# Kernel tuning notes

Hardware: AMD Instinct MI355X
Metric: run time of the kernel (lower is better)

## Reference

```python
import jax, jax.numpy as jnp
import numpy as np

N_EMBD = 1024
N_HEAD = 16
HEAD = N_EMBD // N_HEAD


def setup_inputs() -> dict:
    key = jax.random.key(0)
    ks = jax.random.split(key, 6)
    B, S = 4, 2048
    scale = 1.0 / np.sqrt(N_EMBD)
    return {
        "x": jax.random.normal(ks[0], (B, S, N_EMBD), dtype=jnp.float32),
        "Wq": jax.random.normal(ks[1], (N_EMBD, N_EMBD), dtype=jnp.float32) * scale,
        "Wk": jax.random.normal(ks[2], (N_EMBD, N_EMBD), dtype=jnp.float32) * scale,
        "Wv": jax.random.normal(ks[3], (N_EMBD, N_EMBD), dtype=jnp.float32) * scale,
        "Wo": jax.random.normal(ks[4], (N_EMBD, N_EMBD), dtype=jnp.float32) * scale,
        "bo": jnp.zeros((N_EMBD,), dtype=jnp.float32),
    }


def reference(x, Wq, Wk, Wv, Wo, bo):
    B, S, _ = x.shape
    # projections; nn.Linear applies x @ W.T but W is random here, so x @ W is equivalent math
    def split_heads(t):  # (B,S,E) -> (B,H,S,D)
        return t.reshape(B, S, N_HEAD, HEAD).transpose(0, 2, 1, 3)

    q = split_heads(x @ Wq)
    k = split_heads(x @ Wk)
    v = split_heads(x @ Wv)
    scores = jnp.einsum("bhqd,bhkd->bhqk", q, k) * (HEAD ** -0.5)
    causal = jnp.tril(jnp.ones((S, S), dtype=bool))
    scores = jnp.where(causal, scores, -jnp.inf)
    weights = jax.nn.softmax(scores, axis=-1)  # dropout p=0 (eval)
    out = jnp.einsum("bhqk,bhkd->bhqd", weights, v)
    out = out.transpose(0, 2, 1, 3).reshape(B, S, N_EMBD)
    return out @ Wo + bo
```

## Files before the change

kernel.cpp:

```cpp
#include <hip/hip_runtime.h>
#include <hip/hip_bf16.h>

typedef unsigned short u16;
typedef unsigned int u32;
typedef __bf16 bf16x8 __attribute__((ext_vector_type(8)));
typedef float f32x4 __attribute__((ext_vector_type(4)));
typedef u16 u16x8 __attribute__((ext_vector_type(8)));
typedef u16 u16x4 __attribute__((ext_vector_type(4)));

#define NB 4
#define SEQ 2048
#define EMB 1024
#define NHEAD 16
#define DHEAD 64
#define MTOT (NB*SEQ)

static __device__ __forceinline__ u16 f2bf(float f) {
  union { __bf16 h; u16 u; } cv;
  cv.h = (__bf16)f;
  return cv.u;
}

static __device__ __forceinline__ float fexp2(float x) {
  float r;
  asm("v_exp_f32 %0, %1" : "=v"(r) : "v"(x));
  return r;
}

static __device__ __forceinline__ void gload16(const void* g, void* l) {
  __builtin_amdgcn_global_load_lds((const __attribute__((address_space(1))) void*)g,
                                   (__attribute__((address_space(3))) void*)l, 16, 0, 0);
}


__global__ __launch_bounds__(256) void k_cvt_x(const float* __restrict__ in, u16* __restrict__ out) {
  size_t i = (size_t)blockIdx.x * 256 + threadIdx.x;
  const float4* p = (const float4*)in + i * 2;
  float4 a = p[0], b = p[1];
  u16x8 r;
  r[0] = f2bf(a.x); r[1] = f2bf(a.y); r[2] = f2bf(a.z); r[3] = f2bf(a.w);
  r[4] = f2bf(b.x); r[5] = f2bf(b.y); r[6] = f2bf(b.z); r[7] = f2bf(b.w);
  *(u16x8*)(out + i * 8) = r;
}

__global__ __launch_bounds__(256) void k_wtrans(const float* __restrict__ W0, const float* __restrict__ W1,
                                                const float* __restrict__ W2, const float* __restrict__ W3,
                                                u16* __restrict__ O0, u16* __restrict__ O1,
                                                u16* __restrict__ O2, u16* __restrict__ O3) {
  __shared__ float tile[64][65];
  const float* W = blockIdx.z == 0 ? W0 : blockIdx.z == 1 ? W1 : blockIdx.z == 2 ? W2 : W3;
  u16* O       = blockIdx.z == 0 ? O0 : blockIdx.z == 1 ? O1 : blockIdx.z == 2 ? O2 : O3;
  const int c0 = blockIdx.x * 64, r0 = blockIdx.y * 64;
  const int t = threadIdx.x;
  const int tr = t >> 4, tc = (t & 15) * 4;
#pragma unroll
  for (int p = 0; p < 4; p++) {
    int r = tr + p * 16;
    float4 v = *(const float4*)&W[(size_t)(r0 + r) * EMB + c0 + tc];
    tile[r][tc + 0] = v.x; tile[r][tc + 1] = v.y; tile[r][tc + 2] = v.z; tile[r][tc + 3] = v.w;
  }
  __syncthreads();
#pragma unroll
  for (int p = 0; p < 4; p++) {
    int orow = tr + p * 16;
    u16x4 o;
    o[0] = f2bf(tile[tc + 0][orow]); o[1] = f2bf(tile[tc + 1][orow]);
    o[2] = f2bf(tile[tc + 2][orow]); o[3] = f2bf(tile[tc + 3][orow]);
    *(u16x4*)&O[(size_t)(c0 + orow) * EMB + r0 + tc] = o;
  }
}


static __device__ __forceinline__ void gemm_core(const u16* __restrict__ A, const u16* __restrict__ BT,
                                                 int m0, int n0, f32x4 acc[4][4]) {
  __shared__ u16 As[2][128 * 64];
  __shared__ u16 Bs[2][128 * 64];
  const int t = threadIdx.x, l = t & 63, w = t >> 6;
  const int g = l >> 4, q = l & 15;
  const int wm = (w >> 1) * 64, wn = (w & 1) * 64;

  const f32x4 zero4 = {0.f, 0.f, 0.f, 0.f};
#pragma unroll
  for (int mi = 0; mi < 4; mi++)
#pragma unroll
    for (int ni = 0; ni < 4; ni++) acc[mi][ni] = zero4;

  int srow[4], skel[4];
#pragma unroll
  for (int i = 0; i < 4; i++) {
    int row = w * 32 + i * 8 + (l >> 3);
    srow[i] = row; skel[i] = ((l & 7) ^ (row & 7)) * 8;
  }

  auto stage = [&](int k0, int bsel) {
    char* AsB = (char*)As[bsel] + w * 4096;
    char* BsB = (char*)Bs[bsel] + w * 4096;
#pragma unroll
    for (int i = 0; i < 4; i++) {
      gload16(A + (size_t)(m0 + srow[i]) * EMB + k0 + skel[i], AsB + i * 1024);
      gload16(BT + (size_t)(n0 + srow[i]) * EMB + k0 + skel[i], BsB + i * 1024);
    }
  };

  auto compute = [&](int bsel) {
    char* AsB = (char*)As[bsel];
    char* BsB = (char*)Bs[bsel];
#pragma unroll
    for (int kc = 0; kc < 2; kc++) {
      bf16x8 af[4], bfv[4];
#pragma unroll
      for (int mi = 0; mi < 4; mi++) {
        int row = wm + mi * 16 + q;
        af[mi] = *(const bf16x8*)(AsB + row * 128 + (((kc * 4 + g) ^ (row & 7)) << 4));
      }
#pragma unroll
      for (int ni = 0; ni < 4; ni++) {
        int row = wn + ni * 16 + q;
        bfv[ni] = *(const bf16x8*)(BsB + row * 128 + (((kc * 4 + g) ^ (row & 7)) << 4));
      }
      __builtin_amdgcn_s_setprio(1);
#pragma unroll
      for (int mi = 0; mi < 4; mi++)
#pragma unroll
        for (int ni = 0; ni < 4; ni++)
          acc[mi][ni] = __builtin_amdgcn_mfma_f32_16x16x32_bf16(af[mi], bfv[ni], acc[mi][ni], 0, 0, 0);
      __builtin_amdgcn_s_setprio(0);
    }
  };

  stage(0, 0);
  int buf = 0;
  for (int k0 = 64; k0 <= EMB; k0 += 64) {
    const bool pf = (k0 < EMB);
    if (pf) {
      stage(k0, buf ^ 1);
      asm volatile("s_waitcnt vmcnt(8)" ::: "memory");
    } else {
      asm volatile("s_waitcnt vmcnt(0)" ::: "memory");
    }
    __builtin_amdgcn_s_barrier();
    __builtin_amdgcn_sched_barrier(0);
    compute(buf);
    asm volatile("s_waitcnt lgkmcnt(0)" ::: "memory");
    __builtin_amdgcn_s_barrier();
    buf ^= 1;
  }
}

__global__ __launch_bounds__(512, 2) void k_gemm_qkv(const u16* __restrict__ xb, const u16* __restrict__ Wqkv,
                                                     u16* __restrict__ Qb, u16* __restrict__ Kb, u16* __restrict__ Vb) {
  __shared__ u16 As[2][256 * 64];
  __shared__ u16 Bs[2][256 * 64];
  const int t = threadIdx.x, l = t & 63, wid = t >> 6;
  const int g = l >> 4, q = l & 15;
  const int wr = wid >> 2, wc = wid & 3;

  const int wg = blockIdx.x;
  const int c = wg & 7, local = wg >> 3;
  const int idx = c * 48 + local;
  const int ni_ = idx >> 5, mi_ = idx & 31;
  const int m0 = mi_ * 256, n0 = ni_ * 256;

  f32x4 acc[2][2][4][2];
  const f32x4 zero4 = {0.f, 0.f, 0.f, 0.f};
#pragma unroll
  for (int R = 0; R < 2; R++)
#pragma unroll
    for (int C = 0; C < 2; C++)
#pragma unroll
      for (int mi = 0; mi < 4; mi++)
#pragma unroll
        for (int ni = 0; ni < 2; ni++) acc[R][C][mi][ni] = zero4;

  int srow[2], skel[2];
#pragma unroll
  for (int j = 0; j < 2; j++) {
    int row = j * 64 + (t >> 3);
    srow[j] = row; skel[j] = ((t & 7) ^ (row & 7)) * 8;
  }

  auto stageHalf = [&](int op, int half, int tile) {
    if (tile >= 16) return;
    const int kk = tile * 64, d = tile & 1;
    const u16* src = op ? Wqkv : xb;
    const int base = op ? n0 : m0;
    char* dst = (char*)(op ? Bs[d] : As[d]) + half * 16384 + wid * 1024;
#pragma unroll
    for (int j = 0; j < 2; j++)
      gload16(src + (size_t)(base + half * 128 + srow[j]) * EMB + kk + skel[j], dst + j * 8192);
  };

  bf16x8 af[4][2], bf0[2][2], bf1[2][2];
  auto loadA = [&](int R, int d) {
    char* Ab = (char*)As[d];
#pragma unroll
    for (int mi = 0; mi < 4; mi++)
#pragma unroll
      for (int kc = 0; kc < 2; kc++) {
        int row = R * 128 + wr * 64 + mi * 16 + q;
        af[mi][kc] = *(const bf16x8*)(Ab + row * 128 + (((kc * 4 + g) ^ (row & 7)) << 4));
      }
  };
  auto loadB = [&](int C, int d, bf16x8 (&bfv)[2][2]) {
    char* Bb = (char*)Bs[d];
#pragma unroll
    for (int ni = 0; ni < 2; ni++)
#pragma unroll
      for (int kc = 0; kc < 2; kc++) {
        int row = C * 128 + wc * 32 + ni * 16 + q;
        bfv[ni][kc] = *(const bf16x8*)(Bb + row * 128 + (((kc * 4 + g) ^ (row & 7)) << 4));
      }
  };

#define MFMA16(R, C, BF)                                                                   \
  do {                                                                                     \
    __builtin_amdgcn_s_setprio(1);                                                         \
    _Pragma("unroll")                                                                      \
    for (int kc = 0; kc < 2; kc++)                                                         \
      _Pragma("unroll")                                                                    \
      for (int mi = 0; mi < 4; mi++)                                                       \
        _Pragma("unroll")                                                                  \
        for (int ni = 0; ni < 2; ni++)                                                     \
          acc[R][C][mi][ni] = __builtin_amdgcn_mfma_f32_16x16x32_bf16(af[mi][kc], BF[ni][kc], acc[R][C][mi][ni], 0, 0, 0); \
    __builtin_amdgcn_s_setprio(0);                                                         \
  } while (0)

  stageHalf(0, 0, 0); stageHalf(1, 0, 0); stageHalf(1, 1, 0); stageHalf(0, 1, 0);
  stageHalf(0, 0, 1); stageHalf(1, 1, 1);
  asm volatile("s_waitcnt vmcnt(4)" ::: "memory");
  __builtin_amdgcn_s_barrier();
  __builtin_amdgcn_sched_barrier(0);

  for (int kt = 0; kt < 16; ++kt) {
    const int d = kt & 1;
    loadA(0, d); loadB(0, d, bf0);
    stageHalf(0, 1, kt + 1);
    __builtin_amdgcn_s_barrier();
    MFMA16(0, 0, bf0);
    __builtin_amdgcn_s_barrier();
    __builtin_amdgcn_sched_barrier(0);
    loadB(1, d, bf1);
    stageHalf(1, 0, kt + 1);
    __builtin_amdgcn_s_barrier();
    MFMA16(0, 1, bf1);
    __builtin_amdgcn_s_barrier();
    __builtin_amdgcn_sched_barrier(0);
    loadA(1, d);
    stageHalf(0, 0, kt + 2);
    __builtin_amdgcn_s_barrier();
    MFMA16(1, 1, bf1);
    __builtin_amdgcn_s_barrier();
    __builtin_amdgcn_sched_barrier(0);
    stageHalf(1, 1, kt + 2);
    __builtin_amdgcn_s_barrier();
    MFMA16(1, 0, bf0);
    if (kt <= 13)      asm volatile("s_waitcnt vmcnt(4)" ::: "memory");
    else if (kt == 14) asm volatile("s_waitcnt vmcnt(0)" ::: "memory");
    __builtin_amdgcn_s_barrier();
    __builtin_amdgcn_sched_barrier(0);
  }
#undef MFMA16

  const int z = n0 >> 10;
  u16* Out = z == 0 ? Qb : (z == 1 ? Kb : Vb);
  const float scale = z == 0 ? 0.125f * 1.4426950408889634f : 1.0f;

#pragma unroll
  for (int R = 0; R < 2; R++)
#pragma unroll
    for (int C = 0; C < 2; C++)
#pragma unroll
      for (int mi = 0; mi < 4; mi++)
#pragma unroll
        for (int ni = 0; ni < 2; ni++)
#pragma unroll
          for (int jj = 0; jj < 4; jj++) {
            int m = m0 + R * 128 + wr * 64 + mi * 16 + g * 4 + jj;
            int n = n0 + C * 128 + wc * 32 + ni * 16 + q;
            int b = m >> 11, s = m & 2047;
            int col = n & 1023;
            int h = col >> 6, dd = col & 63;
            Out[(((size_t)(b * NHEAD + h)) * SEQ + s) * DHEAD + dd] = f2bf(acc[R][C][mi][ni][jj] * scale);
          }
}

__global__ __launch_bounds__(256) void k_gemm_out(const u16* __restrict__ Ob, const u16* __restrict__ WoT,
                                                  const float* __restrict__ bo, float* __restrict__ out) {
  const int wg = blockIdx.x;
  const int c = wg & 7, local = wg >> 3;
  const int m0 = (local & 63) * 128, n0 = c * 128;

  f32x4 acc[4][4];
  gemm_core(Ob, WoT, m0, n0, acc);

  const int t = threadIdx.x, l = t & 63, w = t >> 6;
  const int g = l >> 4, q = l & 15;
  const int wm = (w >> 1) * 64, wn = (w & 1) * 64;
#pragma unroll
  for (int ni = 0; ni < 4; ni++) {
    int n = n0 + wn + ni * 16 + q;
    float bv = bo[n];
#pragma unroll
    for (int mi = 0; mi < 4; mi++)
#pragma unroll
      for (int jj = 0; jj < 4; jj++) {
        int m = m0 + wm + mi * 16 + g * 4 + jj;
        out[(size_t)m * EMB + n] = acc[mi][ni][jj] + bv;
      }
  }
}

__global__ __launch_bounds__(256, 4) void k_attn(const u16* __restrict__ Qb, const u16* __restrict__ Kb,
                                                 const u16* __restrict__ Vb, u16* __restrict__ Ob) {
  __shared__ u16 Ks[2][64 * 64];
  __shared__ u16 Vt[2][64 * 64];
  const int t = threadIdx.x, l = t & 63, w = t >> 6;
  const int g = l >> 4, q = l & 15;
  const int bh = blockIdx.x;
  const int b = bh >> 4, h = bh & 15;
  const size_t hb = (size_t)bh * SEQ * DHEAD;
  const float NEG_INF = -__builtin_inff();

  const int i = blockIdx.y;
  const int qA0 = i * 64, qB0 = (31 - i) * 64;
  const int ntA = i + 1, ntB = 32 - i;

  int krow[2], kel[2];
#pragma unroll
  for (int ii = 0; ii < 2; ii++) {
    int row = w * 16 + ii * 8 + (l >> 3);
    krow[ii] = row; kel[ii] = ((l & 7) ^ (row & 7)) * 8;
  }
  const int kp = t & 31, d0v = (t >> 5) * 8;
  const int r2 = 2 * kp;
  const int sp = 32 * ((r2 >> 4) >> 1) + 8 * ((r2 >> 2) & 3) + 4 * ((r2 >> 4) & 1) + (r2 & 3);

  int olds[2][4], owv[8];
#pragma unroll
  for (int kc = 0; kc < 2; kc++)
#pragma unroll
    for (int kf = 0; kf < 4; kf++) {
      int row = kf * 16 + q;
      olds[kc][kf] = row * 128 + (((kc * 4 + g) ^ (row & 7)) << 4);
    }
#pragma unroll
  for (int ii = 0; ii < 8; ii++) {
    int d = d0v + ii;
    owv[ii] = d * 128 + ((sp * 2) ^ ((d & 7) << 4));
  }

  const u16* kgp0 = Kb + hb + (size_t)krow[0] * DHEAD + kel[0];
  const u16* kgp1 = Kb + hb + (size_t)krow[1] * DHEAD + kel[1];
  const u16* vgp0 = Vb + hb + (size_t)(2 * kp) * DHEAD + d0v;
  const u16* vgp1 = vgp0 + DHEAD;

  auto stageK = [&](const u16* p0, const u16* p1, int bsel) {
    char* dst = (char*)Ks[bsel] + w * 2048;
    gload16(p0, dst);
    gload16(p1, dst + 1024);
  };
  auto writeV = [&](int bsel, const u16x8& v0, const u16x8& v1) {
    char* VtB = (char*)Vt[bsel];
#pragma unroll
    for (int ii = 0; ii < 8; ii++) {
      u32 val = (u32)v0[ii] | ((u32)v1[ii] << 16);
      *(u32*)(VtB + owv[ii]) = val;
    }
  };

  bf16x8 qfA[2], qfB[2];
#pragma unroll
  for (int kc = 0; kc < 2; kc++) {
    qfA[kc] = *(const bf16x8*)(Qb + hb + (size_t)(qA0 + w * 16 + q) * DHEAD + kc * 32 + g * 8);
    qfB[kc] = *(const bf16x8*)(Qb + hb + (size_t)(qB0 + w * 16 + q) * DHEAD + kc * 32 + g * 8);
  }
  const int qglobA = qA0 + w * 16 + q, qglobB = qB0 + w * 16 + q;

  f32x4 oA[4], oB[4];
  const f32x4 zero4 = {0.f, 0.f, 0.f, 0.f};
#pragma unroll
  for (int df = 0; df < 4; df++) { oA[df] = zero4; oB[df] = zero4; }
  float mA = NEG_INF, lA = 0.f, mB = NEG_INF, lB = 0.f;

  auto compute = [&](const bf16x8 (&qf)[2], f32x4 (&o)[4], float& m_run, float& l_run,
                     bool diag, int qglob, int k0, const char* KsB, const char* VtB) {
    f32x4 st[4];
#pragma unroll
    for (int kf = 0; kf < 4; kf++) st[kf] = zero4;
    __builtin_amdgcn_s_setprio(1);
#pragma unroll
    for (int kc = 0; kc < 2; kc++)
#pragma unroll
      for (int kf = 0; kf < 4; kf++) {
        bf16x8 a = *(const bf16x8*)(KsB + olds[kc][kf]);
        st[kf] = __builtin_amdgcn_mfma_f32_16x16x32_bf16(a, qf[kc], st[kf], 0, 0, 0);
      }
    __builtin_amdgcn_s_setprio(0);

    if (diag) {
#pragma unroll
      for (int kf = 0; kf < 4; kf++)
#pragma unroll
        for (int jj = 0; jj < 4; jj++)
          if (k0 + kf * 16 + g * 4 + jj > qglob) st[kf][jj] = NEG_INF;
    }

    float x0 = fmaxf(fmaxf(st[0][0], st[0][1]), st[0][2]);
    float x1 = fmaxf(fmaxf(st[0][3], st[1][0]), st[1][1]);
    float x2 = fmaxf(fmaxf(st[1][2], st[1][3]), st[2][0]);
    float x3 = fmaxf(fmaxf(st[2][1], st[2][2]), st[2][3]);
    float x4 = fmaxf(fmaxf(st[3][0], st[3][1]), st[3][2]);
    float smax = fmaxf(fmaxf(x0, x1), x2);
    smax = fmaxf(fmaxf(smax, x3), x4);
    smax = fmaxf(smax, st[3][3]);
    smax = fmaxf(smax, __shfl_xor(smax, 16));
    smax = fmaxf(smax, __shfl_xor(smax, 32));

    if (!__all(smax - m_run <= 8.0f)) {
      float mnew = fmaxf(m_run, smax);
      float sc = fexp2(m_run - mnew);
      l_run *= sc;
#pragma unroll
      for (int jj = 0; jj < 4; jj++) {
        float scj = __shfl(sc, g * 4 + jj);
#pragma unroll
        for (int df = 0; df < 4; df++) o[df][jj] *= scj;
      }
      m_run = mnew;
    }

    f32x4 pv[4];
#pragma unroll
    for (int kf = 0; kf < 4; kf++)
#pragma unroll
      for (int jj = 0; jj < 4; jj++)
        pv[kf][jj] = fexp2(st[kf][jj] - m_run);
    f32x4 sv = (pv[0] + pv[1]) + (pv[2] + pv[3]);
    l_run += (sv[0] + sv[1]) + (sv[2] + sv[3]);

    bf16x8 pa[2];
    pa[0] = bf16x8{ (__bf16)pv[0][0], (__bf16)pv[0][1], (__bf16)pv[0][2], (__bf16)pv[0][3],
                    (__bf16)pv[1][0], (__bf16)pv[1][1], (__bf16)pv[1][2], (__bf16)pv[1][3] };
    pa[1] = bf16x8{ (__bf16)pv[2][0], (__bf16)pv[2][1], (__bf16)pv[2][2], (__bf16)pv[2][3],
                    (__bf16)pv[3][0], (__bf16)pv[3][1], (__bf16)pv[3][2], (__bf16)pv[3][3] };

    __builtin_amdgcn_s_setprio(1);
#pragma unroll
    for (int kc = 0; kc < 2; kc++)
#pragma unroll
      for (int df = 0; df < 4; df++) {
        bf16x8 vb = *(const bf16x8*)(VtB + olds[kc][df]);
        o[df] = __builtin_amdgcn_mfma_f32_16x16x32_bf16(pa[kc], vb, o[df], 0, 0, 0);
      }
    __builtin_amdgcn_s_setprio(0);
  };

  {
    u16x8 v0 = *(const u16x8*)vgp0, v1 = *(const u16x8*)vgp1;
    stageK(kgp0, kgp1, 0);
    writeV(0, v0, v1);
    kgp0 += 4096; kgp1 += 4096; vgp0 += 4096; vgp1 += 4096;
  }
  __syncthreads();

  int buf = 0;
  for (int kt = 0; kt < ntB; ++kt) {
    const int k0 = kt * 64;
    const bool pf = (kt + 1 < ntB);
    u16x8 nv0, nv1;
    if (pf) {
      stageK(kgp0, kgp1, buf ^ 1);
      nv0 = *(const u16x8*)vgp0; nv1 = *(const u16x8*)vgp1;
      kgp0 += 4096; kgp1 += 4096; vgp0 += 4096; vgp1 += 4096;
    }
    const char* KsB = (const char*)Ks[buf];
    const char* VtB = (const char*)Vt[buf];

    compute(qfB, oB, mB, lB, kt == ntB - 1, qglobB, k0, KsB, VtB);
    __builtin_amdgcn_sched_barrier(0);
    if (kt < ntA)
      compute(qfA, oA, mA, lA, kt == ntA - 1, qglobA, k0, KsB, VtB);

    if (pf) writeV(buf ^ 1, nv0, nv1);
    __syncthreads();
    buf ^= 1;
  }

  lA += __shfl_xor(lA, 16); lA += __shfl_xor(lA, 32);
  lB += __shfl_xor(lB, 16); lB += __shfl_xor(lB, 32);

  auto store = [&](f32x4 (&o)[4], float l_run, int q0) {
    float inv = 1.f / l_run;
#pragma unroll
    for (int jj = 0; jj < 4; jj++) {
      float r = __shfl(inv, g * 4 + jj);
      int s = q0 + w * 16 + g * 4 + jj;
#pragma unroll
      for (int df = 0; df < 4; df++)
        Ob[((size_t)(b * SEQ + s)) * EMB + h * DHEAD + df * 16 + q] = f2bf(o[df][jj] * r);
    }
  };
  store(oA, lA, qA0);
  store(oB, lB, qB0);
}


extern "C" void kernel_launch(void* const* d_in, const int* in_sizes, int n_in,
                              void* d_out, int out_size, void* d_ws, size_t ws_size,
                              hipStream_t stream) {
  const float* x  = (const float*)d_in[0];
  const float* Wq = (const float*)d_in[1];
  const float* Wk = (const float*)d_in[2];
  const float* Wv = (const float*)d_in[3];
  const float* Wo = (const float*)d_in[4];
  const float* bo = (const float*)d_in[5];
  float* out = (float*)d_out;

  char* ws = (char*)d_ws;
  u16* xb  = (u16*)(ws);
  u16* WqT = (u16*)(ws + (16u << 20));
  u16* WkT = WqT + (size_t)EMB * EMB;
  u16* WvT = WkT + (size_t)EMB * EMB;
  u16* WoT = WvT + (size_t)EMB * EMB;
  u16* Qb  = (u16*)(ws + (24u << 20));
  u16* Kb  = Qb + (size_t)MTOT * EMB;
  u16* Vb  = Kb + (size_t)MTOT * EMB;
  u16* Ob  = Vb + (size_t)MTOT * EMB;

  k_cvt_x<<<dim3(4096), 256, 0, stream>>>(x, xb);
  k_wtrans<<<dim3(16, 16, 4), 256, 0, stream>>>(Wq, Wk, Wv, Wo, WqT, WkT, WvT, WoT);
  k_gemm_qkv<<<dim3(384), 512, 0, stream>>>(xb, WqT, Qb, Kb, Vb);
  k_attn<<<dim3(64, 16), 256, 0, stream>>>(Qb, Kb, Vb, Ob);
  k_gemm_out<<<dim3(512), 256, 0, stream>>>(Ob, WoT, bo, out);
}
```

Baseline: 165.5 us.

## Share K/V LDS fragment loads across both query blocks in attention loop

Restructures the per-tile attention step so that the QK^T MMAs for both query blocks (A and B) run together using the same K fragments loaded once from LDS. Both softmaxes are then computed, followed by PV MMAs for both blocks using shared V fragments. This halves LDS reads of K/V per tile and interleaves more independent MFMAs. In exchange it raises register pressure, since two sets of score and probability fragments are live at once, and it removes the sched_barrier that separated the two blocks.

```diff
diff --git a/kernel.cpp b/kernel.cpp
--- a/kernel.cpp
+++ b/kernel.cpp
@@ -382,21 +382,8 @@
   for (int df = 0; df < 4; df++) { oA[df] = zero4; oB[df] = zero4; }
   float mA = NEG_INF, lA = 0.f, mB = NEG_INF, lB = 0.f;
 
-  auto compute = [&](const bf16x8 (&qf)[2], f32x4 (&o)[4], float& m_run, float& l_run,
-                     bool diag, int qglob, int k0, const char* KsB, const char* VtB) {
-    f32x4 st[4];
-#pragma unroll
-    for (int kf = 0; kf < 4; kf++) st[kf] = zero4;
-    __builtin_amdgcn_s_setprio(1);
-#pragma unroll
-    for (int kc = 0; kc < 2; kc++)
-#pragma unroll
-      for (int kf = 0; kf < 4; kf++) {
-        bf16x8 a = *(const bf16x8*)(KsB + olds[kc][kf]);
-        st[kf] = __builtin_amdgcn_mfma_f32_16x16x32_bf16(a, qf[kc], st[kf], 0, 0, 0);
-      }
-    __builtin_amdgcn_s_setprio(0);
-
+  auto softmax_pa = [&](f32x4 (&st)[4], f32x4 (&o)[4], float& m_run, float& l_run,
+                        bool diag, int qglob, int k0, bf16x8 (&pa)[2]) {
     if (diag) {
 #pragma unroll
       for (int kf = 0; kf < 4; kf++)
@@ -438,21 +425,10 @@
     f32x4 sv = (pv[0] + pv[1]) + (pv[2] + pv[3]);
     l_run += (sv[0] + sv[1]) + (sv[2] + sv[3]);
 
-    bf16x8 pa[2];
     pa[0] = bf16x8{ (__bf16)pv[0][0], (__bf16)pv[0][1], (__bf16)pv[0][2], (__bf16)pv[0][3],
                     (__bf16)pv[1][0], (__bf16)pv[1][1], (__bf16)pv[1][2], (__bf16)pv[1][3] };
     pa[1] = bf16x8{ (__bf16)pv[2][0], (__bf16)pv[2][1], (__bf16)pv[2][2], (__bf16)pv[2][3],
                     (__bf16)pv[3][0], (__bf16)pv[3][1], (__bf16)pv[3][2], (__bf16)pv[3][3] };
-
-    __builtin_amdgcn_s_setprio(1);
-#pragma unroll
-    for (int kc = 0; kc < 2; kc++)
-#pragma unroll
-      for (int df = 0; df < 4; df++) {
-        bf16x8 vb = *(const bf16x8*)(VtB + olds[kc][df]);
-        o[df] = __builtin_amdgcn_mfma_f32_16x16x32_bf16(pa[kc], vb, o[df], 0, 0, 0);
-      }
-    __builtin_amdgcn_s_setprio(0);
   };
 
   {
@@ -467,6 +443,7 @@
   for (int kt = 0; kt < ntB; ++kt) {
     const int k0 = kt * 64;
     const bool pf = (kt + 1 < ntB);
+    const bool actA = kt < ntA;
     u16x8 nv0, nv1;
     if (pf) {
       stageK(kgp0, kgp1, buf ^ 1);
@@ -476,10 +453,52 @@
     const char* KsB = (const char*)Ks[buf];
     const char* VtB = (const char*)Vt[buf];
 
-    compute(qfB, oB, mB, lB, kt == ntB - 1, qglobB, k0, KsB, VtB);
-    __builtin_amdgcn_sched_barrier(0);
-    if (kt < ntA)
-      compute(qfA, oA, mA, lA, kt == ntA - 1, qglobA, k0, KsB, VtB);
+    f32x4 stB[4], stA[4];
+#pragma unroll
+    for (int kf = 0; kf < 4; kf++) { stB[kf] = zero4; stA[kf] = zero4; }
+#pragma unroll
+    for (int kc = 0; kc < 2; kc++) {
+      bf16x8 k0f = *(const bf16x8*)(KsB + olds[kc][0]);
+      bf16x8 k1f = *(const bf16x8*)(KsB + olds[kc][1]);
+      bf16x8 k2f = *(const bf16x8*)(KsB + olds[kc][2]);
+      bf16x8 k3f = *(const bf16x8*)(KsB + olds[kc][3]);
+      __builtin_amdgcn_s_setprio(1);
+      stB[0] = __builtin_amdgcn_mfma_f32_16x16x32_bf16(k0f, qfB[kc], stB[0], 0, 0, 0);
+      stB[1] = __builtin_amdgcn_mfma_f32_16x16x32_bf16(k1f, qfB[kc], stB[1], 0, 0, 0);
+      stB[2] = __builtin_amdgcn_mfma_f32_16x16x32_bf16(k2f, qfB[kc], stB[2], 0, 0, 0);
+      stB[3] = __builtin_amdgcn_mfma_f32_16x16x32_bf16(k3f, qfB[kc], stB[3], 0, 0, 0);
+      if (actA) {
+        stA[0] = __builtin_amdgcn_mfma_f32_16x16x32_bf16(k0f, qfA[kc], stA[0], 0, 0, 0);
+        stA[1] = __builtin_amdgcn_mfma_f32_16x16x32_bf16(k1f, qfA[kc], stA[1], 0, 0, 0);
+        stA[2] = __builtin_amdgcn_mfma_f32_16x16x32_bf16(k2f, qfA[kc], stA[2], 0, 0, 0);
+        stA[3] = __builtin_amdgcn_mfma_f32_16x16x32_bf16(k3f, qfA[kc], stA[3], 0, 0, 0);
+      }
+      __builtin_amdgcn_s_setprio(0);
+    }
+
+    bf16x8 paB[2], paA[2];
+    softmax_pa(stB, oB, mB, lB, kt == ntB - 1, qglobB, k0, paB);
+    if (actA) softmax_pa(stA, oA, mA, lA, kt == ntA - 1, qglobA, k0, paA);
+
+#pragma unroll
+    for (int kc = 0; kc < 2; kc++) {
+      bf16x8 v0f = *(const bf16x8*)(VtB + olds[kc][0]);
+      bf16x8 v1f = *(const bf16x8*)(VtB + olds[kc][1]);
+      bf16x8 v2f = *(const bf16x8*)(VtB + olds[kc][2]);
+      bf16x8 v3f = *(const bf16x8*)(VtB + olds[kc][3]);
+      __builtin_amdgcn_s_setprio(1);
+      oB[0] = __builtin_amdgcn_mfma_f32_16x16x32_bf16(paB[kc], v0f, oB[0], 0, 0, 0);
+      oB[1] = __builtin_amdgcn_mfma_f32_16x16x32_bf16(paB[kc], v1f, oB[1], 0, 0, 0);
+      oB[2] = __builtin_amdgcn_mfma_f32_16x16x32_bf16(paB[kc], v2f, oB[2], 0, 0, 0);
+      oB[3] = __builtin_amdgcn_mfma_f32_16x16x32_bf16(paB[kc], v3f, oB[3], 0, 0, 0);
+      if (actA) {
+        oA[0] = __builtin_amdgcn_mfma_f32_16x16x32_bf16(paA[kc], v0f, oA[0], 0, 0, 0);
+        oA[1] = __builtin_amdgcn_mfma_f32_16x16x32_bf16(paA[kc], v1f, oA[1], 0, 0, 0);
+        oA[2] = __builtin_amdgcn_mfma_f32_16x16x32_bf16(paA[kc], v2f, oA[2], 0, 0, 0);
+        oA[3] = __builtin_amdgcn_mfma_f32_16x16x32_bf16(paA[kc], v3f, oA[3], 0, 0, 0);
+      }
+      __builtin_amdgcn_s_setprio(0);
+    }
 
     if (pf) writeV(buf ^ 1, nv0, nv1);
     __syncthreads();
```

Result: slower. 253.9 us (+53.4%).
